# Performance work log

Hardware: AMD Instinct MI355X
Metric: run time of the kernel (lower is better)

The kernel has to match this reference:

```python
import jax, jax.numpy as jnp
import numpy as np

LOG_2PI = float(np.log(2.0 * np.pi))


def gaussian_log_density(samples, mean, log_squared_scale):
    inv_sigma = jnp.exp(-log_squared_scale)
    tmp = samples - mean
    return -0.5 * (tmp * tmp * inv_sigma + log_squared_scale + LOG_2PI)


def setup_inputs() -> dict:
    key = jax.random.key(0)
    k1, k2, k3, k4, k5 = jax.random.split(key, 5)
    B, L, D = 4096, 16, 512
    return {
        "data": jax.random.normal(k1, (B, D), dtype=jnp.float32),
        "reconstruction": jax.random.normal(k2, (B, D), dtype=jnp.float32),
        "z": jax.random.normal(k3, (B, L), dtype=jnp.float32),
        "z_mean": jax.random.normal(k4, (B, L), dtype=jnp.float32),
        "z_log_var": jax.random.normal(k5, (B, L), dtype=jnp.float32),
    }


def reference(data, reconstruction, z, z_mean, z_log_var):
    # reconstruction loss: mean over batch of per-sample MAE (mean over feature axis)
    recon_loss = jnp.mean(jnp.abs(data - reconstruction))

    # KL penalty: mean over batch of 0.5 * sum over latents
    summand = jnp.square(z_mean) + jnp.exp(z_log_var) - z_log_var - 1.0
    kl_loss = jnp.mean(0.5 * jnp.sum(summand, axis=1))

    # total correlation: pairwise gaussian log-density [B, B, L]
    log_qz_prob = gaussian_log_density(
        z[:, None, :], z_mean[None, :, :], z_log_var[None, :, :]
    )
    # log prod_l q(z_l): logsumexp over batch axis 1 per latent, then sum over latents
    log_qz_product = jnp.sum(jax.nn.logsumexp(log_qz_prob, axis=1), axis=1)
    # log q(z): sum over latents first, then logsumexp over batch axis
    log_qz = jax.nn.logsumexp(jnp.sum(log_qz_prob, axis=2), axis=1)
    tc_loss = jnp.mean(log_qz - log_qz_product)

    total_loss = recon_loss + kl_loss + tc_loss
    return total_loss
```

## Files before the change

### kernel.cpp

```cpp
#include <hip/hip_runtime.h>
#include <hip/hip_fp16.h>
#include <math.h>

#define BB 4096
#define LL 16
#define DD 512

#define LOG2E_F  1.4426950408889634f
#define LN2_F    0.6931471805599453f
#define LOG2PI_F 1.8378770664093453f

#define OFFC     22.942540f
#define SCALE23  8388608.0f
#define BIASF    126.94269504f

#if __has_builtin(__builtin_amdgcn_exp2f)
#define EXP2(x) __builtin_amdgcn_exp2f(x)
#else
#define EXP2(x) exp2f(x)
#endif
#if __has_builtin(__builtin_amdgcn_logf)
#define LOG2(x) __builtin_amdgcn_logf(x)
#else
#define LOG2(x) log2f(x)
#endif

#define COEF_F   0
#define RP_F     196608
#define KLP_F    198656
#define RED_F    198912
#define PART_F   268544

__device__ __forceinline__ float block_reduce(float v) {
  __shared__ float sm[4];
  __syncthreads();
#pragma unroll
  for (int off = 32; off; off >>= 1) v += __shfl_xor(v, off);
  if ((threadIdx.x & 63) == 0) sm[threadIdx.x >> 6] = v;
  __syncthreads();
  if (threadIdx.x == 0) v = (sm[0] + sm[1]) + (sm[2] + sm[3]);
  return v;
}

__global__ __launch_bounds__(256) void prep_recon_kernel(
    const float4* __restrict__ data4, const float4* __restrict__ recon4,
    const float* __restrict__ zm, const float* __restrict__ zlv,
    float* __restrict__ coef, float* __restrict__ rp,
    float* __restrict__ klp, float* __restrict__ out) {
  const int tid = threadIdx.x;
  const int b = blockIdx.x;

  if (b == 1024 && tid == 0) out[0] = 0.0f;

  {
    const int n4 = (BB * DD) / 4;
    int stride = gridDim.x * 256;
    float s = 0.0f;
    for (int k = b * 256 + tid; k < n4; k += stride) {
      float4 a = data4[k];
      float4 r = recon4[k];
      s += (fabsf(a.x - r.x) + fabsf(a.y - r.y)) +
           (fabsf(a.z - r.z) + fabsf(a.w - r.w));
    }
    float t = block_reduce(s);
    if (tid == 0) rp[b] = t * (1.0f / (float)(BB * DD));
  }

  if (b < 256) {
    const float S = 1024.0f / 65535.0f;
    int idx = b * 256 + tid;
    int j = idx >> 4;
    int l = idx & 15;
    float m = zm[idx];
    float lv = zlv[idx];
    float inv = EXP2(-lv * LOG2E_F);
    float a = -0.5f * LOG2E_F * inv;
    float c2 = -0.5f * LOG2E_F * (lv + LOG2PI_F);
    coef[j * 48 + l]      = a * S;
    coef[j * 48 + 16 + l] = -2.0f * a * m * S;
    coef[j * 48 + 32 + l] = (fmaf(a, m * m, c2) + OFFC) * S;

    float kls = m * m + EXP2(lv * LOG2E_F) - lv - 1.0f;
    float s = block_reduce(kls);
    if (tid == 0) klp[b] = s * (0.5f / (float)BB);
  }
}

template <int CHUNK>
__global__ __launch_bounds__(256, 8) void tc_kernel(
    const float* __restrict__ z, const float* __restrict__ coef,
    float* __restrict__ partial) {
  __shared__ float lcoef[CHUNK * 48];
  const int tid = threadIdx.x;
  const int i = blockIdx.x * 256 + tid;
  const int j0 = blockIdx.y * CHUNK;
  const float JMUL = 65535.0f * 8192.0f;
  const float JK   = -SCALE23 * (16.0f * OFFC - BIASF);

  {
    const float4* g4 = (const float4*)(coef + (size_t)j0 * 48);
    float4* l4 = (float4*)lcoef;
    for (int t = tid; t < (CHUNK * 48) / 4; t += 256) l4[t] = g4[t];
  }

  float zv[16];
  const float4* zp = (const float4*)(z + i * 16);
#pragma unroll
  for (int q = 0; q < 4; ++q) {
    float4 v = zp[q];
    zv[4 * q] = v.x; zv[4 * q + 1] = v.y; zv[4 * q + 2] = v.z; zv[4 * q + 3] = v.w;
  }

  union HU { unsigned u; __half2 h; };
  __half2 accH[8];
#pragma unroll
  for (int p = 0; p < 8; ++p) { HU t; t.u = 0u; accH[p] = t.h; }
  float accJ = 0.0f;

  __syncthreads();

  const float* cp = lcoef;
#pragma unroll 2
  for (int j = 0; j < CHUNK; ++j) {
    float js = 0.0f;
#pragma unroll
    for (int q = 0; q < 4; ++q) {
      float4 va = *(const float4*)(cp + 4 * q);
      float4 vb = *(const float4*)(cp + 16 + 4 * q);
      float4 vc = *(const float4*)(cp + 32 + 4 * q);
      float lp0 = fmaf(fmaf(va.x, zv[4 * q + 0], vb.x), zv[4 * q + 0], vc.x);
      float lp1 = fmaf(fmaf(va.y, zv[4 * q + 1], vb.y), zv[4 * q + 1], vc.y);
      float lp2 = fmaf(fmaf(va.z, zv[4 * q + 2], vb.z), zv[4 * q + 2], vc.z);
      float lp3 = fmaf(fmaf(va.w, zv[4 * q + 3], vb.w), zv[4 * q + 3], vc.w);
      HU t0, t1;
      asm("v_cvt_pknorm_u16_f32 %0, %1, %2"
          : "=v"(t0.u) : "v"(lp0), "v"(lp1));
      asm("v_cvt_pknorm_u16_f32 %0, %1, %2"
          : "=v"(t1.u) : "v"(lp2), "v"(lp3));
      accH[2 * q]     = __hadd2(accH[2 * q], t0.h);
      accH[2 * q + 1] = __hadd2(accH[2 * q + 1], t1.h);
      js += (lp0 + lp1) + (lp2 + lp3);
    }
    float w = fmaf(js, JMUL, JK);
    unsigned u;
    asm("v_cvt_u32_f32 %0, %1" : "=v"(u) : "v"(w));
    accJ += __uint_as_float(u);
    cp += 48;
  }

  float* base = partial + ((size_t)blockIdx.y * 17) * BB + i;
#pragma unroll
  for (int p = 0; p < 8; ++p) {
    base[(size_t)(2 * p) * BB]     = 0.00390625f * __low2float(accH[p]);
    base[(size_t)(2 * p + 1) * BB] = 0.00390625f * __high2float(accH[p]);
  }
  base[(size_t)16 * BB] = accJ;
}

__global__ __launch_bounds__(256) void reduce_kernel(
    const float* __restrict__ partial, float* __restrict__ reduced, int nc) {
  const int i = blockIdx.x * 256 + threadIdx.x;
  const int k = blockIdx.y;
  const float* p = partial + (size_t)k * BB + i;
  const size_t cstride = (size_t)17 * BB;
  float s0 = 0.0f, s1 = 0.0f, s2 = 0.0f, s3 = 0.0f;
  int c = 0;
  for (; c + 4 <= nc; c += 4) {
    s0 += p[(size_t)(c + 0) * cstride];
    s1 += p[(size_t)(c + 1) * cstride];
    s2 += p[(size_t)(c + 2) * cstride];
    s3 += p[(size_t)(c + 3) * cstride];
  }
  for (; c < nc; ++c) s0 += p[(size_t)c * cstride];
  reduced[(size_t)k * BB + i] = (s0 + s1) + (s2 + s3);
}

__global__ __launch_bounds__(256) void final_kernel(
    const float* __restrict__ reduced, const float* __restrict__ rp,
    const float* __restrict__ klp, float* __restrict__ out) {
  const int tid = threadIdx.x;
  const int i = blockIdx.x * 256 + tid;
  float lg = LOG2(reduced[(size_t)16 * BB + i]);
#pragma unroll
  for (int k = 0; k < 16; ++k) lg -= LOG2(reduced[(size_t)k * BB + i]);
  float t = lg * (LN2_F / (float)BB);
  if (blockIdx.x == 0) {
#pragma unroll
    for (int q = 0; q < 8; ++q) t += rp[tid + 256 * q];
    t += klp[tid];
  }
  float s = block_reduce(t);
  if (tid == 0) atomicAdd(out, s);
}

extern "C" void kernel_launch(void* const* d_in, const int* in_sizes, int n_in,
                              void* d_out, int out_size, void* d_ws, size_t ws_size,
                              hipStream_t stream) {
  const float* data  = (const float*)d_in[0];
  const float* recon = (const float*)d_in[1];
  const float* z     = (const float*)d_in[2];
  const float* zm    = (const float*)d_in[3];
  const float* zlv   = (const float*)d_in[4];
  float* out = (float*)d_out;
  float* ws  = (float*)d_ws;

  int nc = 128;
  if (((size_t)PART_F + (size_t)nc * 17 * BB) * 4 > ws_size) nc = 64;

  float* coef = ws + COEF_F;
  float* rp   = ws + RP_F;
  float* klp  = ws + KLP_F;
  float* red  = ws + RED_F;
  float* part = ws + PART_F;

  hipLaunchKernelGGL(prep_recon_kernel, dim3(2048), dim3(256), 0, stream,
                     reinterpret_cast<const float4*>(data),
                     reinterpret_cast<const float4*>(recon),
                     zm, zlv, coef, rp, klp, out);
  if (nc == 128) {
    hipLaunchKernelGGL(tc_kernel<32>, dim3(16, 128), dim3(256), 0, stream,
                       z, coef, part);
  } else {
    hipLaunchKernelGGL(tc_kernel<64>, dim3(16, 64), dim3(256), 0, stream,
                       z, coef, part);
  }
  hipLaunchKernelGGL(reduce_kernel, dim3(BB / 256, 17), dim3(256), 0, stream,
                     part, red, nc);
  hipLaunchKernelGGL(final_kernel, dim3(BB / 256), dim3(256), 0, stream,
                     red, rp, klp, out);
}
```

Measured before the change: 121.6 us.

## Read coefficients directly via uniform loads, reformulate quadratic, halve j-chunks

Drops the LDS staging of per-j coefficients and has each thread read them straight from global memory. Since all lanes share the same address, the compiler can issue scalar loads, which removes the shared-memory copy and the barrier. The log-density is now computed as a*(z-m)^2 + c instead of the expanded polynomial, which is more numerically stable but adds one subtract per element. The chunk size doubles (64 instead of 32 j per block), halving the partial-sum buffer and the reduction work at the cost of fewer blocks in the grid.

```diff
diff --git a/kernel.cpp b/kernel.cpp
--- a/kernel.cpp
+++ b/kernel.cpp
@@ -76,9 +76,9 @@
     float inv = EXP2(-lv * LOG2E_F);
     float a = -0.5f * LOG2E_F * inv;
     float c2 = -0.5f * LOG2E_F * (lv + LOG2PI_F);
-    coef[j * 48 + l]      = a * S;
-    coef[j * 48 + 16 + l] = -2.0f * a * m * S;
-    coef[j * 48 + 32 + l] = (fmaf(a, m * m, c2) + OFFC) * S;
+    coef[j * 48 + l]      = m;
+    coef[j * 48 + 16 + l] = a * S;
+    coef[j * 48 + 32 + l] = (c2 + OFFC) * S;
 
     float kls = m * m + EXP2(lv * LOG2E_F) - lv - 1.0f;
     float s = block_reduce(kls);
@@ -90,19 +90,12 @@
 __global__ __launch_bounds__(256, 8) void tc_kernel(
     const float* __restrict__ z, const float* __restrict__ coef,
     float* __restrict__ partial) {
-  __shared__ float lcoef[CHUNK * 48];
   const int tid = threadIdx.x;
   const int i = blockIdx.x * 256 + tid;
   const int j0 = blockIdx.y * CHUNK;
   const float JMUL = 65535.0f * 8192.0f;
   const float JK   = -SCALE23 * (16.0f * OFFC - BIASF);
 
-  {
-    const float4* g4 = (const float4*)(coef + (size_t)j0 * 48);
-    float4* l4 = (float4*)lcoef;
-    for (int t = tid; t < (CHUNK * 48) / 4; t += 256) l4[t] = g4[t];
-  }
-
   float zv[16];
   const float4* zp = (const float4*)(z + i * 16);
 #pragma unroll
@@ -117,28 +110,34 @@
   for (int p = 0; p < 8; ++p) { HU t; t.u = 0u; accH[p] = t.h; }
   float accJ = 0.0f;
 
-  __syncthreads();
-
-  const float* cp = lcoef;
+  const float* cp = coef + (size_t)j0 * 48;
 #pragma unroll 2
   for (int j = 0; j < CHUNK; ++j) {
     float js = 0.0f;
 #pragma unroll
     for (int q = 0; q < 4; ++q) {
-      float4 va = *(const float4*)(cp + 4 * q);
-      float4 vb = *(const float4*)(cp + 16 + 4 * q);
-      float4 vc = *(const float4*)(cp + 32 + 4 * q);
-      float lp0 = fmaf(fmaf(va.x, zv[4 * q + 0], vb.x), zv[4 * q + 0], vc.x);
-      float lp1 = fmaf(fmaf(va.y, zv[4 * q + 1], vb.y), zv[4 * q + 1], vc.y);
-      float lp2 = fmaf(fmaf(va.z, zv[4 * q + 2], vb.z), zv[4 * q + 2], vc.z);
-      float lp3 = fmaf(fmaf(va.w, zv[4 * q + 3], vb.w), zv[4 * q + 3], vc.w);
-      HU t0, t1;
+      float4 m4 = *(const float4*)(cp + 4 * q);
+      float4 a4 = *(const float4*)(cp + 16 + 4 * q);
+      float4 c4 = *(const float4*)(cp + 32 + 4 * q);
+      float t0 = zv[4 * q + 0] - m4.x;
+      float t1 = zv[4 * q + 1] - m4.y;
+      float t2 = zv[4 * q + 2] - m4.z;
+      float t3 = zv[4 * q + 3] - m4.w;
+      float u0 = a4.x * t0;
+      float u1 = a4.y * t1;
+      float u2 = a4.z * t2;
+      float u3 = a4.w * t3;
+      float lp0 = fmaf(u0, t0, c4.x);
+      float lp1 = fmaf(u1, t1, c4.y);
+      float lp2 = fmaf(u2, t2, c4.z);
+      float lp3 = fmaf(u3, t3, c4.w);
+      HU t0h, t1h;
       asm("v_cvt_pknorm_u16_f32 %0, %1, %2"
-          : "=v"(t0.u) : "v"(lp0), "v"(lp1));
+          : "=v"(t0h.u) : "v"(lp0), "v"(lp1));
       asm("v_cvt_pknorm_u16_f32 %0, %1, %2"
-          : "=v"(t1.u) : "v"(lp2), "v"(lp3));
-      accH[2 * q]     = __hadd2(accH[2 * q], t0.h);
-      accH[2 * q + 1] = __hadd2(accH[2 * q + 1], t1.h);
+          : "=v"(t1h.u) : "v"(lp2), "v"(lp3));
+      accH[2 * q]     = __hadd2(accH[2 * q], t0h.h);
+      accH[2 * q + 1] = __hadd2(accH[2 * q + 1], t1h.h);
       js += (lp0 + lp1) + (lp2 + lp3);
     }
     float w = fmaf(js, JMUL, JK);
@@ -204,8 +203,8 @@
   float* out = (float*)d_out;
   float* ws  = (float*)d_ws;
 
-  int nc = 128;
-  if (((size_t)PART_F + (size_t)nc * 17 * BB) * 4 > ws_size) nc = 64;
+  int nc = 64;
+  if (((size_t)PART_F + (size_t)nc * 17 * BB) * 4 > ws_size) nc = 32;
 
   float* coef = ws + COEF_F;
   float* rp   = ws + RP_F;
@@ -217,11 +216,11 @@
                      reinterpret_cast<const float4*>(data),
                      reinterpret_cast<const float4*>(recon),
                      zm, zlv, coef, rp, klp, out);
-  if (nc == 128) {
-    hipLaunchKernelGGL(tc_kernel<32>, dim3(16, 128), dim3(256), 0, stream,
+  if (nc == 64) {
+    hipLaunchKernelGGL(tc_kernel<64>, dim3(16, 64), dim3(256), 0, stream,
                        z, coef, part);
   } else {
-    hipLaunchKernelGGL(tc_kernel<64>, dim3(16, 64), dim3(256), 0, stream,
+    hipLaunchKernelGGL(tc_kernel<128>, dim3(16, 32), dim3(256), 0, stream,
                        z, coef, part);
   }
   hipLaunchKernelGGL(reduce_kernel, dim3(BB / 256, 17), dim3(256), 0, stream,
```

New measurement: 128.7 us. 1.06x slower.

## Register-block four rows per thread in TC kernel and use centered quadratic form

Applied to the files above, without the earlier changes.

Each thread in the total-correlation kernel now processes four z rows, so every coefficient vector loaded from shared memory is reused four times, and the grid shrinks accordingly. The coefficient layout stores the mean, scaled inverse variance and constant, and the log-density is evaluated as a*(z-m)^2+c. This targets LDS bandwidth and instruction overhead per pair, at the cost of more registers and far fewer resident waves, which may expose latency.

```diff
diff --git a/kernel.cpp b/kernel.cpp
--- a/kernel.cpp
+++ b/kernel.cpp
@@ -76,9 +76,9 @@
     float inv = EXP2(-lv * LOG2E_F);
     float a = -0.5f * LOG2E_F * inv;
     float c2 = -0.5f * LOG2E_F * (lv + LOG2PI_F);
-    coef[j * 48 + l]      = a * S;
-    coef[j * 48 + 16 + l] = -2.0f * a * m * S;
-    coef[j * 48 + 32 + l] = (fmaf(a, m * m, c2) + OFFC) * S;
+    coef[j * 48 + l]      = m;
+    coef[j * 48 + 16 + l] = a * S;
+    coef[j * 48 + 32 + l] = (c2 + OFFC) * S;
 
     float kls = m * m + EXP2(lv * LOG2E_F) - lv - 1.0f;
     float s = block_reduce(kls);
@@ -87,12 +87,12 @@
 }
 
 template <int CHUNK>
-__global__ __launch_bounds__(256, 8) void tc_kernel(
+__global__ __launch_bounds__(256, 2) void tc_kernel(
     const float* __restrict__ z, const float* __restrict__ coef,
     float* __restrict__ partial) {
   __shared__ float lcoef[CHUNK * 48];
   const int tid = threadIdx.x;
-  const int i = blockIdx.x * 256 + tid;
+  const int i0 = blockIdx.x * 1024 + tid;
   const int j0 = blockIdx.y * CHUNK;
   const float JMUL = 65535.0f * 8192.0f;
   const float JK   = -SCALE23 * (16.0f * OFFC - BIASF);
@@ -103,58 +103,77 @@
     for (int t = tid; t < (CHUNK * 48) / 4; t += 256) l4[t] = g4[t];
   }
 
-  float zv[16];
-  const float4* zp = (const float4*)(z + i * 16);
-#pragma unroll
-  for (int q = 0; q < 4; ++q) {
-    float4 v = zp[q];
-    zv[4 * q] = v.x; zv[4 * q + 1] = v.y; zv[4 * q + 2] = v.z; zv[4 * q + 3] = v.w;
+  float zv[4][16];
+#pragma unroll
+  for (int r = 0; r < 4; ++r) {
+    const float4* zp = (const float4*)(z + (size_t)(i0 + 256 * r) * 16);
+#pragma unroll
+    for (int q = 0; q < 4; ++q) {
+      float4 v = zp[q];
+      zv[r][4 * q] = v.x; zv[r][4 * q + 1] = v.y;
+      zv[r][4 * q + 2] = v.z; zv[r][4 * q + 3] = v.w;
+    }
   }
 
   union HU { unsigned u; __half2 h; };
-  __half2 accH[8];
-#pragma unroll
-  for (int p = 0; p < 8; ++p) { HU t; t.u = 0u; accH[p] = t.h; }
-  float accJ = 0.0f;
+  __half2 accH[4][8];
+#pragma unroll
+  for (int r = 0; r < 4; ++r)
+#pragma unroll
+    for (int p = 0; p < 8; ++p) { HU t; t.u = 0u; accH[r][p] = t.h; }
+  float accJ[4] = {0.0f, 0.0f, 0.0f, 0.0f};
 
   __syncthreads();
 
   const float* cp = lcoef;
 #pragma unroll 2
   for (int j = 0; j < CHUNK; ++j) {
-    float js = 0.0f;
+    float js[4] = {0.0f, 0.0f, 0.0f, 0.0f};
 #pragma unroll
     for (int q = 0; q < 4; ++q) {
-      float4 va = *(const float4*)(cp + 4 * q);
-      float4 vb = *(const float4*)(cp + 16 + 4 * q);
-      float4 vc = *(const float4*)(cp + 32 + 4 * q);
-      float lp0 = fmaf(fmaf(va.x, zv[4 * q + 0], vb.x), zv[4 * q + 0], vc.x);
-      float lp1 = fmaf(fmaf(va.y, zv[4 * q + 1], vb.y), zv[4 * q + 1], vc.y);
-      float lp2 = fmaf(fmaf(va.z, zv[4 * q + 2], vb.z), zv[4 * q + 2], vc.z);
-      float lp3 = fmaf(fmaf(va.w, zv[4 * q + 3], vb.w), zv[4 * q + 3], vc.w);
-      HU t0, t1;
-      asm("v_cvt_pknorm_u16_f32 %0, %1, %2"
-          : "=v"(t0.u) : "v"(lp0), "v"(lp1));
-      asm("v_cvt_pknorm_u16_f32 %0, %1, %2"
-          : "=v"(t1.u) : "v"(lp2), "v"(lp3));
-      accH[2 * q]     = __hadd2(accH[2 * q], t0.h);
-      accH[2 * q + 1] = __hadd2(accH[2 * q + 1], t1.h);
-      js += (lp0 + lp1) + (lp2 + lp3);
-    }
-    float w = fmaf(js, JMUL, JK);
-    unsigned u;
-    asm("v_cvt_u32_f32 %0, %1" : "=v"(u) : "v"(w));
-    accJ += __uint_as_float(u);
+      float4 m4 = *(const float4*)(cp + 4 * q);
+      float4 a4 = *(const float4*)(cp + 16 + 4 * q);
+      float4 c4 = *(const float4*)(cp + 32 + 4 * q);
+#pragma unroll
+      for (int r = 0; r < 4; ++r) {
+        float t0 = zv[r][4 * q + 0] - m4.x;
+        float t1 = zv[r][4 * q + 1] - m4.y;
+        float t2 = zv[r][4 * q + 2] - m4.z;
+        float t3 = zv[r][4 * q + 3] - m4.w;
+        float lp0 = fmaf(a4.x * t0, t0, c4.x);
+        float lp1 = fmaf(a4.y * t1, t1, c4.y);
+        float lp2 = fmaf(a4.z * t2, t2, c4.z);
+        float lp3 = fmaf(a4.w * t3, t3, c4.w);
+        HU h0, h1;
+        asm("v_cvt_pknorm_u16_f32 %0, %1, %2"
+            : "=v"(h0.u) : "v"(lp0), "v"(lp1));
+        asm("v_cvt_pknorm_u16_f32 %0, %1, %2"
+            : "=v"(h1.u) : "v"(lp2), "v"(lp3));
+        accH[r][2 * q]     = __hadd2(accH[r][2 * q], h0.h);
+        accH[r][2 * q + 1] = __hadd2(accH[r][2 * q + 1], h1.h);
+        js[r] += (lp0 + lp1) + (lp2 + lp3);
+      }
+    }
+#pragma unroll
+    for (int r = 0; r < 4; ++r) {
+      float w = fmaf(js[r], JMUL, JK);
+      unsigned u;
+      asm("v_cvt_u32_f32 %0, %1" : "=v"(u) : "v"(w));
+      accJ[r] += __uint_as_float(u);
+    }
     cp += 48;
   }
 
-  float* base = partial + ((size_t)blockIdx.y * 17) * BB + i;
-#pragma unroll
-  for (int p = 0; p < 8; ++p) {
-    base[(size_t)(2 * p) * BB]     = 0.00390625f * __low2float(accH[p]);
-    base[(size_t)(2 * p + 1) * BB] = 0.00390625f * __high2float(accH[p]);
-  }
-  base[(size_t)16 * BB] = accJ;
+#pragma unroll
+  for (int r = 0; r < 4; ++r) {
+    float* base = partial + ((size_t)blockIdx.y * 17) * BB + (i0 + 256 * r);
+#pragma unroll
+    for (int p = 0; p < 8; ++p) {
+      base[(size_t)(2 * p) * BB]     = 0.00390625f * __low2float(accH[r][p]);
+      base[(size_t)(2 * p + 1) * BB] = 0.00390625f * __high2float(accH[r][p]);
+    }
+    base[(size_t)16 * BB] = accJ[r];
+  }
 }
 
 __global__ __launch_bounds__(256) void reduce_kernel(
@@ -218,10 +237,10 @@
                      reinterpret_cast<const float4*>(recon),
                      zm, zlv, coef, rp, klp, out);
   if (nc == 128) {
-    hipLaunchKernelGGL(tc_kernel<32>, dim3(16, 128), dim3(256), 0, stream,
+    hipLaunchKernelGGL(tc_kernel<32>, dim3(4, 128), dim3(256), 0, stream,
                        z, coef, part);
   } else {
-    hipLaunchKernelGGL(tc_kernel<64>, dim3(16, 64), dim3(256), 0, stream,
+    hipLaunchKernelGGL(tc_kernel<64>, dim3(4, 64), dim3(256), 0, stream,
                        z, coef, part);
   }
   hipLaunchKernelGGL(reduce_kernel, dim3(BB / 256, 17), dim3(256), 0, stream,
```

Measured after the change: 125.2 us. +3.0%, slower.
